# Kernel optimization log

Hardware: AMD Instinct MI355X
Metric: run time of the kernel (lower is better)

Reference implementation:

```python
import jax, jax.numpy as jnp
import numpy as np

GAMMA = 0.1
IN_FEATURES = 256 * 2048  # flattened per-sample size
K = int(GAMMA * IN_FEATURES)  # 52428


def setup_inputs() -> dict:
    key = jax.random.key(0)
    x = jax.random.normal(key, (64, 256, 2048), dtype=jnp.float32)
    return {"x": x}


def reference(x) -> jnp.ndarray:
    # Flatten each sample: [B, D1*D2]
    b = x.shape[0]
    tmpx = x.reshape(b, -1)
    # k-th largest value per row (torch.topk returns sorted descending; [:, -1] is k-th largest)
    topval = jax.lax.top_k(tmpx, K)[0][:, -1]  # [B]
    topval = topval.reshape(-1, 1, 1)  # broadcast over [B, D1, D2]
    # Faithful to original: mask keeps values strictly BELOW the threshold (topval > x)
    out = jnp.where(topval > x, x, jnp.zeros((), dtype=x.dtype))
    return out
```

## Files before the change

kernel.cpp:

```cpp
#include <hip/hip_runtime.h>
#include <stdint.h>

constexpr int ROWS = 64;
constexpr int D = 1 << 19;
constexpr uint32_t KSEL = 52428;
constexpr int BPR = 32;
constexpr int CHUNK = D / BPR;
constexpr int LBUF = 896;
constexpr uint32_t PRED_B = 0xBFAu;

constexpr int FBPR = 64;
constexpr int FCHUNK_V4 = (D / 4) / FBPR;

constexpr size_t OFF_SCNT  = 0;
constexpr size_t OFF_ACNT  = 2048;
constexpr size_t OFF_THR   = 4096;
constexpr size_t OFF_CHIST = 4160;
constexpr size_t OFF_KEYS  = OFF_CHIST + 2048 * 512;

typedef float f32x4 __attribute__((ext_vector_type(4)));

__device__ __forceinline__ uint32_t mono(uint32_t f) {
    uint32_t m = (uint32_t)((int32_t)f >> 31) | 0x80000000u;
    return f ^ m;
}

__global__ __launch_bounds__(256) void cand_scan(const uint32_t* __restrict__ x,
                                                 uint32_t* __restrict__ ws) {
    __shared__ uint32_t lkey[LBUF];
    __shared__ uint32_t h1[1024];
    __shared__ uint32_t red[256];
    __shared__ uint32_t ln;
    for (int i = threadIdx.x; i < 1024; i += 256) h1[i] = 0;
    if (threadIdx.x == 0) ln = 0;
    __syncthreads();
    const int bid = blockIdx.x;
    const int row = bid / BPR, chunk = bid % BPR, t = threadIdx.x;
    const uint4* __restrict__ p = (const uint4*)(x + (size_t)row * D + (size_t)chunk * CHUNK);
    uint32_t above = 0;
    for (int i = t; i < CHUNK / 4; i += 256) {
        uint4 v = p[i];
#define CLS(comp)                                                          \
        {                                                                  \
            uint32_t u = mono(comp);                                       \
            uint32_t bu = u >> 20;                                         \
            above += (bu > PRED_B);                                        \
            if (bu == PRED_B) {                                            \
                uint32_t s = atomicAdd(&ln, 1u);                           \
                if (s < (uint32_t)LBUF) lkey[s] = u;                       \
                atomicAdd(&h1[(u >> 10) & 0x3FFu], 1u);                    \
            }                                                              \
        }
        CLS(v.x) CLS(v.y) CLS(v.z) CLS(v.w)
#undef CLS
    }
    red[t] = above;
    __syncthreads();
    for (int off = 128; off > 0; off >>= 1) {
        if (t < off) red[t] += red[t + off];
        __syncthreads();
    }
    if (t == 0) {
        ws[OFF_SCNT + bid] = ln;
        ws[OFF_ACNT + bid] = red[0];
    }
    {
        uint32_t* ch = ws + OFF_CHIST + (size_t)bid * 512;
        for (int i = t; i < 512; i += 256)
            ch[i] = (h1[2 * i] & 0xFFFFu) | (h1[2 * i + 1] << 16);
    }
    uint32_t m = ln < (uint32_t)LBUF ? ln : (uint32_t)LBUF;
    uint32_t* sk = ws + OFF_KEYS + (size_t)bid * LBUF;
    for (uint32_t i = t; i < m; i += 256) sk[i] = lkey[i];
}

__global__ __launch_bounds__(256) void select_thr(const uint32_t* __restrict__ x,
                                                  uint32_t* __restrict__ ws) {
    __shared__ uint32_t h[1024];
    __shared__ uint32_t sc[256];
    __shared__ uint32_t cnts[BPR];
    __shared__ uint32_t bc[2];
    const int row = blockIdx.x, t = threadIdx.x;

    uint32_t myc = 0, mya = 0;
    if (t < BPR) {
        myc = ws[OFF_SCNT + (size_t)row * BPR + t];
        mya = ws[OFF_ACNT + (size_t)row * BPR + t];
        cnts[t] = myc < (uint32_t)LBUF ? myc : (uint32_t)LBUF;
    }
    sc[t] = (t < BPR) ? ((myc > (uint32_t)LBUF ? 0x40000000u : 0u) + myc) : 0u;
    __syncthreads();
    for (int off = 128; off > 0; off >>= 1) {
        if (t < off) sc[t] += sc[t + off];
        __syncthreads();
    }
    const uint32_t ntot_f = sc[0];
    __syncthreads();
    sc[t] = (t < BPR) ? mya : 0u;
    __syncthreads();
    for (int off = 128; off > 0; off >>= 1) {
        if (t < off) sc[t] += sc[t + off];
        __syncthreads();
    }
    const uint32_t above = sc[0];
    const uint32_t n = ntot_f & 0x3FFFFFFFu;
    const bool valid = ((ntot_f & 0xC0000000u) == 0u) &&
                       (above < KSEL) && (above + n >= KSEL);
    __syncthreads();

    if (valid) {
        const uint32_t k = KSEL - above;

        const int base_bin = 1020 - 4 * t;
        uint32_t acc[4] = {0, 0, 0, 0};
        const uint32_t* ch0 = ws + OFF_CHIST + (size_t)row * BPR * 512 + (base_bin >> 1);
#pragma unroll 4
        for (int s = 0; s < BPR; ++s) {
            uint32_t p0 = ch0[(size_t)s * 512];
            uint32_t p1 = ch0[(size_t)s * 512 + 1];
            acc[0] += p0 & 0xFFFFu; acc[1] += p0 >> 16;
            acc[2] += p1 & 0xFFFFu; acc[3] += p1 >> 16;
        }
        uint32_t s_sum = acc[0] + acc[1] + acc[2] + acc[3];
        sc[t] = s_sum;
        __syncthreads();
        for (int off = 1; off < 256; off <<= 1) {
            uint32_t v = (t >= off) ? sc[t - off] : 0u;
            __syncthreads();
            sc[t] += v;
            __syncthreads();
        }
        uint32_t excl = sc[t] - s_sum;
        if (excl < k && excl + s_sum >= k) {
            uint32_t cc = excl;
            for (int j = 3; j >= 0; --j) {
                cc += acc[j];
                if (cc >= k) {
                    bc[0] = (uint32_t)(base_bin + j);
                    bc[1] = k - (cc - acc[j]);
                    break;
                }
            }
        }
        __syncthreads();
        const uint32_t b1 = bc[0], k2 = bc[1];
        __syncthreads();

        for (int i = t; i < 1024; i += 256) h[i] = 0;
        __syncthreads();
        const uint32_t* keys0 = ws + OFF_KEYS + (size_t)row * BPR * LBUF;
        const uint32_t total_slots = BPR * LBUF;
        for (uint32_t g = t; g < total_slots; g += 256) {
            uint32_t seg = g / (uint32_t)LBUF;
            uint32_t i = g - seg * (uint32_t)LBUF;
            if (i < cnts[seg]) {
                uint32_t u = keys0[g];
                if (((u >> 10) & 0x3FFu) == b1) atomicAdd(&h[u & 0x3FFu], 1u);
            }
        }
        __syncthreads();
        {
            int hi = 1023 - t * 4;
            uint32_t s = 0;
            for (int j = 0; j < 4; ++j) s += h[hi - j];
            sc[t] = s;
            __syncthreads();
            for (int off = 1; off < 256; off <<= 1) {
                uint32_t v = (t >= off) ? sc[t - off] : 0u;
                __syncthreads();
                sc[t] += v;
                __syncthreads();
            }
            uint32_t excl2 = sc[t] - s;
            if (excl2 < k2 && excl2 + s >= k2) {
                uint32_t cc = excl2;
                for (int j = 0; j < 4; ++j) {
                    int bin = hi - j;
                    uint32_t hb = h[bin];
                    cc += hb;
                    if (cc >= k2) {
                        ws[OFF_THR + row] = (PRED_B << 20) | (b1 << 10) | (uint32_t)bin;
                        break;
                    }
                }
            }
        }
        return;
    }

    const uint4* px = (const uint4*)(x + (size_t)row * D);
    for (int i = t; i < 1024; i += 256) h[i] = 0;
    __syncthreads();
    for (int i = t; i < D / 4; i += 256) {
        uint4 v = px[i];
        atomicAdd(&h[mono(v.x) >> 22], 1u);
        atomicAdd(&h[mono(v.y) >> 22], 1u);
        atomicAdd(&h[mono(v.z) >> 22], 1u);
        atomicAdd(&h[mono(v.w) >> 22], 1u);
    }
    __syncthreads();
    {
        int hi = 1023 - t * 4;
        uint32_t s = 0;
        for (int j = 0; j < 4; ++j) s += h[hi - j];
        sc[t] = s;
        __syncthreads();
        for (int off = 1; off < 256; off <<= 1) {
            uint32_t v = (t >= off) ? sc[t - off] : 0u;
            __syncthreads();
            sc[t] += v;
            __syncthreads();
        }
        uint32_t excl = sc[t] - s;
        if (excl < KSEL && excl + s >= KSEL) {
            uint32_t cc = excl;
            for (int j = 0; j < 4; ++j) {
                int bin = hi - j;
                uint32_t hb = h[bin];
                cc += hb;
                if (cc >= KSEL) { bc[0] = (uint32_t)bin; bc[1] = KSEL - (cc - hb); break; }
            }
        }
    }
    __syncthreads();
    const uint32_t B10 = bc[0], r1 = bc[1];
    __syncthreads();
    for (int i = t; i < 1024; i += 256) h[i] = 0;
    __syncthreads();
    for (int i = t; i < D / 4; i += 256) {
        uint4 v = px[i];
        uint32_t u;
        u = mono(v.x); if ((u >> 22) == B10) atomicAdd(&h[(u >> 12) & 0x3FFu], 1u);
        u = mono(v.y); if ((u >> 22) == B10) atomicAdd(&h[(u >> 12) & 0x3FFu], 1u);
        u = mono(v.z); if ((u >> 22) == B10) atomicAdd(&h[(u >> 12) & 0x3FFu], 1u);
        u = mono(v.w); if ((u >> 22) == B10) atomicAdd(&h[(u >> 12) & 0x3FFu], 1u);
    }
    __syncthreads();
    {
        int hi = 1023 - t * 4;
        uint32_t s = 0;
        for (int j = 0; j < 4; ++j) s += h[hi - j];
        sc[t] = s;
        __syncthreads();
        for (int off = 1; off < 256; off <<= 1) {
            uint32_t v = (t >= off) ? sc[t - off] : 0u;
            __syncthreads();
            sc[t] += v;
            __syncthreads();
        }
        uint32_t excl = sc[t] - s;
        if (excl < r1 && excl + s >= r1) {
            uint32_t cc = excl;
            for (int j = 0; j < 4; ++j) {
                int bin = hi - j;
                uint32_t hb = h[bin];
                cc += hb;
                if (cc >= r1) { bc[0] = (uint32_t)bin; bc[1] = r1 - (cc - hb); break; }
            }
        }
    }
    __syncthreads();
    const uint32_t pref20 = (B10 << 10) | bc[0];
    const uint32_t r2 = bc[1];
    __syncthreads();
    for (int i = t; i < 1024; i += 256) h[i] = 0;
    __syncthreads();
    for (int i = t; i < D / 4; i += 256) {
        uint4 v = px[i];
        uint32_t u;
        u = mono(v.x); if ((u >> 12) == pref20) atomicAdd(&h[(u >> 2) & 0x3FFu], 1u);
        u = mono(v.y); if ((u >> 12) == pref20) atomicAdd(&h[(u >> 2) & 0x3FFu], 1u);
        u = mono(v.z); if ((u >> 12) == pref20) atomicAdd(&h[(u >> 2) & 0x3FFu], 1u);
        u = mono(v.w); if ((u >> 12) == pref20) atomicAdd(&h[(u >> 2) & 0x3FFu], 1u);
    }
    __syncthreads();
    {
        int hi = 1023 - t * 4;
        uint32_t s = 0;
        for (int j = 0; j < 4; ++j) s += h[hi - j];
        sc[t] = s;
        __syncthreads();
        for (int off = 1; off < 256; off <<= 1) {
            uint32_t v = (t >= off) ? sc[t - off] : 0u;
            __syncthreads();
            sc[t] += v;
            __syncthreads();
        }
        uint32_t excl = sc[t] - s;
        if (excl < r2 && excl + s >= r2) {
            uint32_t cc = excl;
            for (int j = 0; j < 4; ++j) {
                int bin = hi - j;
                uint32_t hb = h[bin];
                cc += hb;
                if (cc >= r2) { bc[0] = (pref20 << 10) | (uint32_t)bin; bc[1] = r2 - (cc - hb); break; }
            }
        }
    }
    __syncthreads();
    const uint32_t pref30 = bc[0];
    const uint32_t r3 = bc[1];
    __syncthreads();
    if (t < 4) h[t] = 0;
    __syncthreads();
    for (int i = t; i < D / 4; i += 256) {
        uint4 v = px[i];
        uint32_t u;
        u = mono(v.x); if ((u >> 2) == pref30) atomicAdd(&h[u & 3u], 1u);
        u = mono(v.y); if ((u >> 2) == pref30) atomicAdd(&h[u & 3u], 1u);
        u = mono(v.z); if ((u >> 2) == pref30) atomicAdd(&h[u & 3u], 1u);
        u = mono(v.w); if ((u >> 2) == pref30) atomicAdd(&h[u & 3u], 1u);
    }
    __syncthreads();
    if (t == 0) {
        uint32_t cc = 0;
        for (int b = 3; b >= 0; --b) {
            cc += h[b];
            if (cc >= r3) { ws[OFF_THR + row] = (pref30 << 2) | (uint32_t)b; break; }
        }
    }
}

__global__ __launch_bounds__(256) void mask_final(const uint32_t* __restrict__ x,
                                                  float* __restrict__ out,
                                                  const uint32_t* __restrict__ ws) {
    const int bid = blockIdx.x;
    const int row = bid / FBPR, chunk = bid % FBPR, t = threadIdx.x;
    const uint32_t tk = ws[OFF_THR + row];
    const uint4* __restrict__ p =
        (const uint4*)(x + (size_t)row * D) + (size_t)chunk * FCHUNK_V4;
    f32x4* __restrict__ o =
        (f32x4*)(out + (size_t)row * D) + (size_t)chunk * FCHUNK_V4;

    uint4 v[8];
#pragma unroll
    for (int k = 0; k < 8; ++k) v[k] = p[t + k * 256];
    f32x4 ov[8];
#pragma unroll
    for (int k = 0; k < 8; ++k) {
        ov[k][0] = (mono(v[k].x) < tk) ? __uint_as_float(v[k].x) : 0.0f;
        ov[k][1] = (mono(v[k].y) < tk) ? __uint_as_float(v[k].y) : 0.0f;
        ov[k][2] = (mono(v[k].z) < tk) ? __uint_as_float(v[k].z) : 0.0f;
        ov[k][3] = (mono(v[k].w) < tk) ? __uint_as_float(v[k].w) : 0.0f;
    }
#pragma unroll
    for (int k = 0; k < 8; ++k)
        __builtin_nontemporal_store(ov[k], &o[t + k * 256]);
}

extern "C" void kernel_launch(void* const* d_in, const int* in_sizes, int n_in,
                              void* d_out, int out_size, void* d_ws, size_t ws_size,
                              hipStream_t stream) {
    (void)in_sizes; (void)n_in; (void)out_size; (void)ws_size;
    const uint32_t* xu = (const uint32_t*)d_in[0];
    float* outp = (float*)d_out;
    uint32_t* ws = (uint32_t*)d_ws;

    cand_scan<<<ROWS * BPR, 256, 0, stream>>>(xu, ws);
    select_thr<<<ROWS, 256, 0, stream>>>(xu, ws);
    mask_final<<<ROWS * FBPR, 256, 0, stream>>>(xu, outp, ws);
}
```

Before: 95.54 us.

## Bucket candidate keys by sub-bin so selection scans only the matching bucket

In cand_scan, each block's candidate keys are counting-sorted in shared memory into 32 buckets by bits 15..19 and the per-bucket counts are written to the workspace. select_thr then reads those counts and, for each segment, scans only the bucket containing the chosen first-level bin instead of every stored candidate slot. This trades extra shared-memory sorting work and one more workspace array in the scan kernel for far fewer global reads in the per-row selection kernel, which runs on only 64 blocks.

```diff
diff --git a/kernel.cpp b/kernel.cpp
--- a/kernel.cpp
+++ b/kernel.cpp
@@ -15,7 +15,8 @@
 constexpr size_t OFF_SCNT  = 0;
 constexpr size_t OFF_ACNT  = 2048;
 constexpr size_t OFF_THR   = 4096;
-constexpr size_t OFF_CHIST = 4160;
+constexpr size_t OFF_BCNT  = 4160;
+constexpr size_t OFF_CHIST = OFF_BCNT + 2048 * 32;
 constexpr size_t OFF_KEYS  = OFF_CHIST + 2048 * 512;
 
 typedef float f32x4 __attribute__((ext_vector_type(4)));
@@ -28,10 +29,13 @@
 __global__ __launch_bounds__(256) void cand_scan(const uint32_t* __restrict__ x,
                                                  uint32_t* __restrict__ ws) {
     __shared__ uint32_t lkey[LBUF];
+    __shared__ uint32_t lkey2[LBUF];
     __shared__ uint32_t h1[1024];
     __shared__ uint32_t red[256];
+    __shared__ uint32_t bcnt[32], bpre[32], boff[32];
     __shared__ uint32_t ln;
     for (int i = threadIdx.x; i < 1024; i += 256) h1[i] = 0;
+    if (threadIdx.x < 32) { bcnt[threadIdx.x] = 0; boff[threadIdx.x] = 0; }
     if (threadIdx.x == 0) ln = 0;
     __syncthreads();
     const int bid = blockIdx.x;
@@ -64,21 +68,36 @@
         ws[OFF_SCNT + bid] = ln;
         ws[OFF_ACNT + bid] = red[0];
     }
+    const uint32_t m = ln < (uint32_t)LBUF ? ln : (uint32_t)LBUF;
+    for (uint32_t i = t; i < m; i += 256) atomicAdd(&bcnt[(lkey[i] >> 15) & 31u], 1u);
+    __syncthreads();
+    if (t == 0) {
+        uint32_t a = 0;
+        for (int b = 0; b < 32; ++b) { bpre[b] = a; a += bcnt[b]; }
+    }
+    __syncthreads();
+    for (uint32_t i = t; i < m; i += 256) {
+        uint32_t u = lkey[i];
+        uint32_t b = (u >> 15) & 31u;
+        uint32_t pos = bpre[b] + atomicAdd(&boff[b], 1u);
+        lkey2[pos] = u;
+    }
+    __syncthreads();
+    if (t < 32) ws[OFF_BCNT + (size_t)bid * 32 + t] = bcnt[t];
     {
         uint32_t* ch = ws + OFF_CHIST + (size_t)bid * 512;
         for (int i = t; i < 512; i += 256)
             ch[i] = (h1[2 * i] & 0xFFFFu) | (h1[2 * i + 1] << 16);
     }
-    uint32_t m = ln < (uint32_t)LBUF ? ln : (uint32_t)LBUF;
     uint32_t* sk = ws + OFF_KEYS + (size_t)bid * LBUF;
-    for (uint32_t i = t; i < m; i += 256) sk[i] = lkey[i];
+    for (uint32_t i = t; i < m; i += 256) sk[i] = lkey2[i];
 }
 
 __global__ __launch_bounds__(256) void select_thr(const uint32_t* __restrict__ x,
                                                   uint32_t* __restrict__ ws) {
     __shared__ uint32_t h[1024];
     __shared__ uint32_t sc[256];
-    __shared__ uint32_t cnts[BPR];
+    __shared__ uint32_t segbase[BPR], segcnt[BPR];
     __shared__ uint32_t bc[2];
     const int row = blockIdx.x, t = threadIdx.x;
 
@@ -86,7 +105,6 @@
     if (t < BPR) {
         myc = ws[OFF_SCNT + (size_t)row * BPR + t];
         mya = ws[OFF_ACNT + (size_t)row * BPR + t];
-        cnts[t] = myc < (uint32_t)LBUF ? myc : (uint32_t)LBUF;
     }
     sc[t] = (t < BPR) ? ((myc > (uint32_t)LBUF ? 0x40000000u : 0u) + myc) : 0u;
     __syncthreads();
@@ -146,15 +164,26 @@
         const uint32_t b1 = bc[0], k2 = bc[1];
         __syncthreads();
 
+        const uint32_t sb = b1 >> 5;
+        if (t < BPR) {
+            const uint32_t* bc_ = ws + OFF_BCNT + ((size_t)row * BPR + t) * 32;
+            uint32_t a = 0, c = 0;
+            for (uint32_t b = 0; b < 32; ++b) {
+                uint32_t v = bc_[b];
+                if (b < sb) a += v;
+                if (b == sb) c = v;
+            }
+            segbase[t] = a;
+            segcnt[t] = c;
+        }
         for (int i = t; i < 1024; i += 256) h[i] = 0;
         __syncthreads();
         const uint32_t* keys0 = ws + OFF_KEYS + (size_t)row * BPR * LBUF;
-        const uint32_t total_slots = BPR * LBUF;
-        for (uint32_t g = t; g < total_slots; g += 256) {
-            uint32_t seg = g / (uint32_t)LBUF;
-            uint32_t i = g - seg * (uint32_t)LBUF;
-            if (i < cnts[seg]) {
-                uint32_t u = keys0[g];
+        for (int seg = 0; seg < BPR; ++seg) {
+            uint32_t c = segcnt[seg];
+            const uint32_t* sk = keys0 + (size_t)seg * LBUF + segbase[seg];
+            for (uint32_t i = t; i < c; i += 256) {
+                uint32_t u = sk[i];
                 if (((u >> 10) & 0x3FFu) == b1) atomicAdd(&h[u & 0x3FFu], 1u);
             }
         }
```

Measured after the change: 88.59 us. 1.08x faster.
